# Optimization experiments

Measured on AMD Instinct MI355X. Metric: run time of the kernel, lower is better.

## Reference

```python
import jax, jax.numpy as jnp
import numpy as np

B, T, C, H, D, G, V, M = 4, 1024, 768, 12, 4, 4, 32000, 1024
S = C // H


def layernorm(x, g, b, eps=1e-5):
    mu = jnp.mean(x, -1, keepdims=True)
    var = jnp.mean(jnp.square(x - mu), -1, keepdims=True)
    return (x - mu) * jax.lax.rsqrt(var + eps) * g + b


def setup_inputs() -> dict:
    key = jax.random.key(0)
    ks = jax.random.split(key, 12)
    std = 0.02  # matches _init_weights normal(0, 0.02)
    n = lambda k, sh: jax.random.normal(k, sh, jnp.float32) * std
    return {
        'x': jax.random.randint(ks[0], (B, T), 0, V),
        'y': jax.random.randint(ks[1], (B, T), 0, V),
        'wordemb': n(ks[2], (V, C)),
        'posemb': n(ks[3], (M, C)),
        'Wq': n(ks[4], (D, C, C)),
        'Wk': n(ks[5], (D, C, C)),
        'Wv': n(ks[6], (D, C, C)),
        'Wo': n(ks[7], (D, C, C)),
        'bo': jnp.zeros((D, C), jnp.float32),
        'ln1_g': jnp.ones((D, C), jnp.float32),
        'ln1_b': jnp.zeros((D, C), jnp.float32),
        'W1': n(ks[8], (D, C, G * C)),
        'b1': jnp.zeros((D, G * C), jnp.float32),
        'W2': n(ks[9], (D, G * C, C)),
        'b2': jnp.zeros((D, C), jnp.float32),
        'ln2_g': jnp.ones((D, C), jnp.float32),
        'ln2_b': jnp.zeros((D, C), jnp.float32),
        'Wl': n(ks[10], (C, V)),
        'bl': jnp.zeros((V,), jnp.float32),
    }


def _forward(x, y, wordemb, posemb, Wq, Wk, Wv, Wo, bo, ln1_g, ln1_b,
             W1, b1, W2, b2, ln2_g, ln2_b, Wl, bl):
    b, t = x.shape
    emb = wordemb[x] + posemb[:t][None, :, :]  # (b,t,c)
    causal = jnp.tril(jnp.ones((t, t), bool))

    def block(h_in, p):
        wq, wk, wv, wo, bo_, g1, be1, w1, b1_, w2, b2_, g2, be2 = p
        q = (h_in @ wq).reshape(b, t, H, S)
        k = (h_in @ wk).reshape(b, t, H, S)
        v = (h_in @ wv).reshape(b, t, H, S)
        # note: original scales by sqrt(channels), NOT sqrt(head_dim)
        w = jnp.einsum('bqhs,bkhs->bhqk', q, k) / jnp.sqrt(jnp.float32(C))
        w = jnp.where(causal, w, -jnp.inf)
        w = jax.nn.softmax(w, axis=-1)
        att = jnp.einsum('bhqk,bkhs->bqhs', w, v).reshape(b, t, C)
        att = att @ wo + bo_
        h1 = h_in + layernorm(att, g1, be1)   # x + norm1(attn(x))
        ff = jax.nn.relu(h1 @ w1 + b1_) @ w2 + b2_
        h2 = h1 + layernorm(ff, g2, be2)      # x + norm2(ff(x)); dropout=0
        return h2, None

    hfin, _ = jax.lax.scan(
        block, emb,
        (Wq, Wk, Wv, Wo, bo, ln1_g, ln1_b, W1, b1, W2, b2, ln2_g, ln2_b))
    logits = hfin @ Wl + bl  # (b,t,v)
    logp = jax.nn.log_softmax(logits, axis=-1)
    nll = -jnp.take_along_axis(logp, y[..., None], axis=-1)[..., 0]
    loss = jnp.mean(nll)
    return logits, loss


def reference(x, y, wordemb, posemb, Wq, Wk, Wv, Wo, bo, ln1_g, ln1_b,
              W1, b1, W2, b2, ln2_g, ln2_b, Wl, bl):
    return _forward(x, y, wordemb, posemb, Wq, Wk, Wv, Wo, bo, ln1_g, ln1_b,
                    W1, b1, W2, b2, ln2_g, ln2_b, Wl, bl)
```

## Files before the change

kernel.cpp:

```cpp
#include <hip/hip_runtime.h>

#define Bn 4
#define Tn 1024
#define Cn 768
#define Hn 12
#define Dn 4
#define Vn 32000
#define BTn (Bn*Tn)
#define NBX 125

typedef __attribute__((ext_vector_type(8))) short short8;
typedef __attribute__((ext_vector_type(4))) float f32x4;

__device__ __forceinline__ unsigned short f2bf(float f) {
  union { float f; unsigned u; } v; v.f = f;
  unsigned r = v.u + 0x7fffu + ((v.u >> 16) & 1u);
  return (unsigned short)(r >> 16);
}

__device__ __forceinline__ void gload_lds16(const void* g, void* l) {
  __builtin_amdgcn_global_load_lds(
      (const __attribute__((address_space(1))) void*)g,
      (__attribute__((address_space(3))) void*)l, 16, 0, 0);
}

__global__ __launch_bounds__(256)
void transpose_bf16_kernel(const float* __restrict__ src0, unsigned short* __restrict__ dst0,
                           int K, int N, size_t sStride, size_t dStride) {
  const float* src = src0 + blockIdx.z * sStride;
  unsigned short* dst = dst0 + blockIdx.z * dStride;
  __shared__ float tile[32][33];
  const int tx = threadIdx.x, ty = threadIdx.y;
  const int n0 = blockIdx.x * 32, k0 = blockIdx.y * 32;
#pragma unroll
  for (int i = 0; i < 4; ++i)
    tile[ty + i*8][tx] = src[(size_t)(k0 + ty + i*8) * N + n0 + tx];
  __syncthreads();
#pragma unroll
  for (int i = 0; i < 4; ++i)
    dst[(size_t)(n0 + ty + i*8) * K + k0 + tx] = f2bf(tile[tx][ty + i*8]);
}

__global__ __launch_bounds__(256)
void embed_kernel(const int* __restrict__ x, const float* __restrict__ wordemb,
                  const float* __restrict__ posemb, float* __restrict__ h,
                  unsigned short* __restrict__ hb) {
  int i4 = blockIdx.x * 256 + threadIdx.x;
  int row = i4 / (Cn/4), c4 = i4 % (Cn/4);
  int t = row & (Tn - 1);
  int tok = x[row];
  float4 a = ((const float4*)wordemb)[(size_t)tok * (Cn/4) + c4];
  float4 p = ((const float4*)posemb)[(size_t)t * (Cn/4) + c4];
  float4 s; s.x = a.x+p.x; s.y = a.y+p.y; s.z = a.z+p.z; s.w = a.w+p.w;
  ((float4*)h)[i4] = s;
  ushort4 u; u.x = f2bf(s.x); u.y = f2bf(s.y); u.z = f2bf(s.z); u.w = f2bf(s.w);
  ((ushort4*)hb)[i4] = u;
}

__global__ __launch_bounds__(256, 2)
void gemm_l(const unsigned short* __restrict__ A, const unsigned short* __restrict__ Bt,
            const float* __restrict__ bias, float* __restrict__ Cf,
            unsigned short* __restrict__ Cb, int M, int N, int K, int relu) {
  __shared__ __align__(16) unsigned short lds[2*16384];
  const int tid = threadIdx.x;
  const int gx = gridDim.x;
  const int flat = blockIdx.x + gx*blockIdx.y;
  const int chq = (gx * gridDim.y) >> 3;
  const int swz = (flat & 7)*chq + (flat >> 3);
  const int by = swz % gx, bx = swz / gx;
  const int lane = tid & 63, w = tid >> 6;
  const int wr = w >> 1, wc = w & 1;
  const int lr = lane & 15, lq = lane >> 4;
  const int xm = (lr >> 1) & 3;
  const int sslot = (lane & 3) ^ ((lane >> 3) & 3);
  const int NT = K >> 6;

  f32x4 acc[4][4];
#pragma unroll
  for (int i = 0; i < 4; ++i)
#pragma unroll
    for (int j = 0; j < 4; ++j)
      acc[i][j] = (f32x4){0.f, 0.f, 0.f, 0.f};

  const unsigned short* aS = A  + (size_t)(by*128 + w*16 + (lane>>2))*K + sslot*8;
  const unsigned short* bS = Bt + (size_t)(bx*128 + w*16 + (lane>>2))*K + sslot*8;

  auto stA = [&](int t) {
    unsigned short* d = &lds[(t&1)*16384];
    const int k0 = t*64;
#pragma unroll
    for (int kh = 0; kh < 2; ++kh)
#pragma unroll
      for (int i = 0; i < 2; ++i)
        gload_lds16(aS + k0 + kh*32 + (size_t)i*64*K, d + kh*4096 + (i*64 + w*16)*32);
  };
  auto stB = [&](int t) {
    unsigned short* d = &lds[(t&1)*16384 + 8192];
    const int k0 = t*64;
#pragma unroll
    for (int kh = 0; kh < 2; ++kh)
#pragma unroll
      for (int i = 0; i < 2; ++i)
        gload_lds16(bS + k0 + kh*32 + (size_t)i*64*K, d + kh*4096 + (i*64 + w*16)*32);
  };
  auto rdA = [&](int t, int kh, short8* af) {
    const unsigned short* p = &lds[(t&1)*16384 + kh*4096];
#pragma unroll
    for (int mi = 0; mi < 4; ++mi)
      af[mi] = *(const short8*)&p[(wr*64 + mi*16 + lr)*32 + (lq ^ xm)*8];
  };
  auto rdB = [&](int t, int kh, short8* bf) {
    const unsigned short* p = &lds[(t&1)*16384 + 8192 + kh*4096];
#pragma unroll
    for (int nj = 0; nj < 4; ++nj)
      bf[nj] = *(const short8*)&p[(wc*64 + nj*16 + lr)*32 + (lq ^ xm)*8];
  };

  short8 af0[4], af1[4], bf0[4], bf1[4];
  stA(0); stB(0); stA(1);

  for (int t = 0; t < NT; ++t) {
    if (t + 1 < NT) { asm volatile("s_waitcnt vmcnt(4)" ::: "memory"); }
    else            { asm volatile("s_waitcnt vmcnt(0)" ::: "memory"); }
    __builtin_amdgcn_s_barrier();
    __builtin_amdgcn_sched_barrier(0);
    rdA(t, 0, af0); rdA(t, 1, af1); rdB(t, 0, bf0);
    if (t + 1 < NT) stB(t + 1);
    __builtin_amdgcn_s_barrier();
    __builtin_amdgcn_sched_barrier(0);
    __builtin_amdgcn_s_setprio(1);
#pragma unroll
    for (int i = 0; i < 4; ++i)
#pragma unroll
      for (int j = 0; j < 4; ++j)
        acc[i][j] = __builtin_amdgcn_mfma_f32_16x16x32_bf16(af0[i], bf0[j], acc[i][j], 0, 0, 0);
    __builtin_amdgcn_s_setprio(0);
    __builtin_amdgcn_s_barrier();
    rdB(t, 1, bf1);
    if (t + 2 < NT) stA(t + 2);
    __builtin_amdgcn_s_barrier();
    __builtin_amdgcn_sched_barrier(0);
    __builtin_amdgcn_s_setprio(1);
#pragma unroll
    for (int i = 0; i < 4; ++i)
#pragma unroll
      for (int j = 0; j < 4; ++j)
        acc[i][j] = __builtin_amdgcn_mfma_f32_16x16x32_bf16(af1[i], bf1[j], acc[i][j], 0, 0, 0);
    __builtin_amdgcn_s_setprio(0);
  }

#pragma unroll
  for (int mi = 0; mi < 4; ++mi)
#pragma unroll
    for (int nj = 0; nj < 4; ++nj)
#pragma unroll
      for (int r = 0; r < 4; ++r) {
        int grow = by*128 + wr*64 + mi*16 + lq*4 + r;
        int gcol = bx*128 + wc*64 + nj*16 + lr;
        float v = acc[mi][nj][r];
        if (bias) v += bias[gcol];
        if (relu) v = fmaxf(v, 0.f);
        size_t idx = (size_t)grow * N + gcol;
        if (Cf) Cf[idx] = v;
        if (Cb) Cb[idx] = f2bf(v);
      }
}

__global__ __launch_bounds__(512, 1)
void gemm_vocab(const unsigned short* __restrict__ A, const unsigned short* __restrict__ Bt,
                const float* __restrict__ bias, float* __restrict__ Cf,
                float2* __restrict__ lsepart) {
  constexpr int K = 768, N = Vn, NT = 12;
  __shared__ __align__(16) unsigned short lds[2*32768];
  const int tid = threadIdx.x;
  const int bid = blockIdx.x;
  const int swz = (bid & 7)*250 + (bid >> 3);
  const int by = swz & 15, bx = swz >> 4;
  const int lane = tid & 63, w = tid >> 6;
  const int wr = w >> 2, wc = w & 3;
  const int lr = lane & 15, lq = lane >> 4;
  const int xm = (lr >> 1) & 3;
  const int sslot = (lane & 3) ^ ((lane >> 3) & 3);

  f32x4 accLo[4][4], accHi[4][4];
#pragma unroll
  for (int i = 0; i < 4; ++i)
#pragma unroll
    for (int j = 0; j < 4; ++j) {
      accLo[i][j] = (f32x4){0.f,0.f,0.f,0.f};
      accHi[i][j] = (f32x4){0.f,0.f,0.f,0.f};
    }

  const unsigned short* aS = A  + (size_t)(by*256 + w*16 + (lane>>2))*K + sslot*8;
  const unsigned short* bS = Bt + (size_t)(bx*256 + w*16 + (lane>>2))*K + sslot*8;

  auto stA = [&](int t) {
    unsigned short* d = &lds[(t&1)*32768];
    const int k0 = t*64;
#pragma unroll
    for (int kh = 0; kh < 2; ++kh)
#pragma unroll
      for (int i = 0; i < 2; ++i)
        gload_lds16(aS + k0 + kh*32 + (size_t)i*128*K, d + kh*8192 + (i*128 + w*16)*32);
  };
  auto stB = [&](int t) {
    unsigned short* d = &lds[(t&1)*32768 + 16384];
    const int k0 = t*64;
#pragma unroll
    for (int kh = 0; kh < 2; ++kh)
#pragma unroll
      for (int i = 0; i < 2; ++i)
        gload_lds16(bS + k0 + kh*32 + (size_t)i*128*K, d + kh*8192 + (i*128 + w*16)*32);
  };
  auto rdA = [&](int t, int kh, int mh, short8* af) {
    const unsigned short* p = &lds[(t&1)*32768 + kh*8192];
#pragma unroll
    for (int mi = 0; mi < 4; ++mi)
      af[mi] = *(const short8*)&p[(wr*128 + mh*64 + mi*16 + lr)*32 + (lq ^ xm)*8];
  };
  auto rdB = [&](int t, int kh, short8* bf) {
    const unsigned short* p = &lds[(t&1)*32768 + 16384 + kh*8192];
#pragma unroll
    for (int nj = 0; nj < 4; ++nj)
      bf[nj] = *(const short8*)&p[(wc*64 + nj*16 + lr)*32 + (lq ^ xm)*8];
  };

  short8 aLo0[4], aHi0[4], aLo1[4], aHi1[4], bf0[4], bf1[4];
  stA(0); stB(0); stA(1); stB(1);

  for (int t = 0; t < NT; ++t) {
    if (t + 1 < NT) { asm volatile("s_waitcnt vmcnt(8)" ::: "memory"); }
    else            { asm volatile("s_waitcnt vmcnt(0)" ::: "memory"); }
    __builtin_amdgcn_s_barrier();
    __builtin_amdgcn_sched_barrier(0);
    rdA(t, 0, 0, aLo0); rdA(t, 0, 1, aHi0); rdB(t, 0, bf0);
    __builtin_amdgcn_s_barrier();
    __builtin_amdgcn_sched_barrier(0);
    __builtin_amdgcn_s_setprio(1);
#pragma unroll
    for (int i = 0; i < 4; ++i)
#pragma unroll
      for (int j = 0; j < 4; ++j)
        accLo[i][j] = __builtin_amdgcn_mfma_f32_16x16x32_bf16(aLo0[i], bf0[j], accLo[i][j], 0, 0, 0);
    __builtin_amdgcn_s_setprio(0);
    __builtin_amdgcn_s_barrier();
    rdA(t, 1, 0, aLo1); rdA(t, 1, 1, aHi1);
    __builtin_amdgcn_s_barrier();
    __builtin_amdgcn_sched_barrier(0);
    __builtin_amdgcn_s_setprio(1);
#pragma unroll
    for (int i = 0; i < 4; ++i)
#pragma unroll
      for (int j = 0; j < 4; ++j)
        accHi[i][j] = __builtin_amdgcn_mfma_f32_16x16x32_bf16(aHi0[i], bf0[j], accHi[i][j], 0, 0, 0);
    __builtin_amdgcn_s_setprio(0);
    __builtin_amdgcn_s_barrier();
    rdB(t, 1, bf1);
    if (t + 2 < NT) stA(t + 2);
    __builtin_amdgcn_s_barrier();
    __builtin_amdgcn_sched_barrier(0);
    __builtin_amdgcn_s_setprio(1);
#pragma unroll
    for (int i = 0; i < 4; ++i)
#pragma unroll
      for (int j = 0; j < 4; ++j)
        accLo[i][j] = __builtin_amdgcn_mfma_f32_16x16x32_bf16(aLo1[i], bf1[j], accLo[i][j], 0, 0, 0);
    __builtin_amdgcn_s_setprio(0);
    __builtin_amdgcn_s_barrier();
    if (t + 2 < NT) stB(t + 2);
    __builtin_amdgcn_s_barrier();
    __builtin_amdgcn_sched_barrier(0);
    __builtin_amdgcn_s_setprio(1);
#pragma unroll
    for (int i = 0; i < 4; ++i)
#pragma unroll
      for (int j = 0; j < 4; ++j)
        accHi[i][j] = __builtin_amdgcn_mfma_f32_16x16x32_bf16(aHi1[i], bf1[j], accHi[i][j], 0, 0, 0);
    __builtin_amdgcn_s_setprio(0);
  }

  float2* part = (float2*)lds;
#pragma unroll
  for (int half = 0; half < 2; ++half) {
#pragma unroll
    for (int mi = 0; mi < 4; ++mi)
#pragma unroll
      for (int r = 0; r < 4; ++r) {
        float v[4]; float m = -3.0e38f;
#pragma unroll
        for (int nj = 0; nj < 4; ++nj) {
          int gcol = bx*256 + wc*64 + nj*16 + lr;
          float val = (half ? accHi[mi][nj][r] : accLo[mi][nj][r]) + bias[gcol];
          v[nj] = val;
          m = fmaxf(m, val);
        }
        int prow = wr*128 + half*64 + mi*16 + lq*4 + r;
        int grow = by*256 + prow;
        float* crow = Cf + (size_t)grow * N + bx*256 + wc*64 + lr;
#pragma unroll
        for (int nj = 0; nj < 4; ++nj) crow[nj*16] = v[nj];
        float s = 0.f;
#pragma unroll
        for (int nj = 0; nj < 4; ++nj) s += __expf(v[nj] - m);
#pragma unroll
        for (int mask = 1; mask < 16; mask <<= 1) {
          float m2 = __shfl_xor(m, mask), s2 = __shfl_xor(s, mask);
          float mn = fmaxf(m, m2);
          s = s*__expf(m - mn) + s2*__expf(m2 - mn);
          m = mn;
        }
        if (lr == 0) part[prow*4 + wc] = make_float2(m, s);
      }
  }
  __syncthreads();
  if (tid < 256) {
    float2 p = part[tid*4];
    float m = p.x, s = p.y;
#pragma unroll
    for (int wcc = 1; wcc < 4; ++wcc) {
      float2 p2 = part[tid*4 + wcc];
      float mn = fmaxf(m, p2.x);
      s = s*__expf(m - mn) + p2.y*__expf(p2.x - mn);
      m = mn;
    }
    lsepart[(size_t)(by*256 + tid)*NBX + bx] = make_float2(m, s);
  }
}

__global__ __launch_bounds__(256)
void vT_kernel(const unsigned short* __restrict__ qkvb, unsigned short* __restrict__ vT) {
  const int tb = blockIdx.x, hh = blockIdx.y, b = blockIdx.z;
  const int t = threadIdx.x;
  __shared__ unsigned short tile[64][65];
  const int r = t >> 2, c = t & 3;
  const unsigned short* src = qkvb + (size_t)(b*Tn + tb*64 + r) * 2304 + 1536 + hh*64 + c*16;
  short8 v0 = *(const short8*)src;
  short8 v1 = *(const short8*)(src + 8);
#pragma unroll
  for (int j = 0; j < 8; ++j) { tile[r][c*16 + j] = (unsigned short)v0[j]; tile[r][c*16 + 8 + j] = (unsigned short)v1[j]; }
  __syncthreads();
  unsigned short o[16];
#pragma unroll
  for (int j = 0; j < 16; ++j) o[j] = tile[c*16 + j][r];
  unsigned short* dst = vT + ((size_t)((b*Hn + hh)*64 + r)) * Tn + tb*64 + c*16;
  *(ushort4*)(dst)      = *(ushort4*)&o[0];
  *(ushort4*)(dst + 4)  = *(ushort4*)&o[4];
  *(ushort4*)(dst + 8)  = *(ushort4*)&o[8];
  *(ushort4*)(dst + 12) = *(ushort4*)&o[12];
}

__global__ __launch_bounds__(256)
void attn_mfma_kernel(const unsigned short* __restrict__ qkvb,
                      const unsigned short* __restrict__ vT,
                      unsigned short* __restrict__ attb) {
  const int qb = blockIdx.x, hh = blockIdx.y, b = blockIdx.z;
  const int t = threadIdx.x;
  const int lane = t & 63, w = t >> 6;
  const int lr = lane & 15, lg = lane >> 4;
  const float scale = 0.03608439182435161f;

  __shared__ unsigned short Ks[64*64];
  __shared__ unsigned short Vs[64*64];
  __shared__ unsigned short Ps[4][16][72];

  const unsigned short* qsrc = qkvb + (size_t)(b*Tn + qb*64 + w*16 + lr)*2304 + hh*64 + lg*8;
  short8 qa0 = *(const short8*)(qsrc);
  short8 qa1 = *(const short8*)(qsrc + 32);

  f32x4 acc[4];
#pragma unroll
  for (int dt = 0; dt < 4; ++dt) acc[dt] = (f32x4){0.f,0.f,0.f,0.f};
  float m_run[4], l_run[4];
#pragma unroll
  for (int r = 0; r < 4; ++r) { m_run[r] = -1e30f; l_run[r] = 0.f; }

  const int sr = t >> 2, c2 = t & 3;

  for (int kvb = 0; kvb <= qb; ++kvb) {
    __syncthreads();
    {
      const unsigned short* ksrc = qkvb + (size_t)(b*Tn + kvb*64 + sr)*2304 + 768 + hh*64 + c2*16;
      short8 k0 = *(const short8*)ksrc;
      short8 k1 = *(const short8*)(ksrc + 8);
      const unsigned short* vsrc = vT + ((size_t)((b*Hn + hh)*64 + sr))*Tn + kvb*64 + c2*16;
      short8 vv0 = *(const short8*)vsrc;
      short8 vv1 = *(const short8*)(vsrc + 8);
      int s0 = (2*c2) ^ (sr & 7), s1 = (2*c2 + 1) ^ (sr & 7);
      *(short8*)&Ks[sr*64 + s0*8] = k0;
      *(short8*)&Ks[sr*64 + s1*8] = k1;
      *(short8*)&Vs[sr*64 + s0*8] = vv0;
      *(short8*)&Vs[sr*64 + s1*8] = vv1;
    }
    __syncthreads();

    f32x4 s[4];
#pragma unroll
    for (int kt = 0; kt < 4; ++kt) {
      int krow = kt*16 + lr;
      short8 kf0 = *(const short8*)&Ks[krow*64 + ((0 + lg) ^ (krow & 7))*8];
      short8 kf1 = *(const short8*)&Ks[krow*64 + ((4 + lg) ^ (krow & 7))*8];
      f32x4 a = (f32x4){0.f,0.f,0.f,0.f};
      a = __builtin_amdgcn_mfma_f32_16x16x32_bf16(qa0, kf0, a, 0, 0, 0);
      a = __builtin_amdgcn_mfma_f32_16x16x32_bf16(qa1, kf1, a, 0, 0, 0);
      s[kt] = a;
    }
    const bool diag = (kvb == qb);
#pragma unroll
    for (int kt = 0; kt < 4; ++kt)
#pragma unroll
      for (int r = 0; r < 4; ++r) {
        float v = s[kt][r] * scale;
        if (diag && (kt*16 + lr > w*16 + lg*4 + r)) v = -1e30f;
        s[kt][r] = v;
      }
#pragma unroll
    for (int r = 0; r < 4; ++r) {
      float m = fmaxf(fmaxf(s[0][r], s[1][r]), fmaxf(s[2][r], s[3][r]));
      m = fmaxf(m, __shfl_xor(m, 1));
      m = fmaxf(m, __shfl_xor(m, 2));
      m = fmaxf(m, __shfl_xor(m, 4));
      m = fmaxf(m, __shfl_xor(m, 8));
      float mn = fmaxf(m_run[r], m);
      float corr = __expf(m_run[r] - mn);
      m_run[r] = mn;
      float ps = 0.f;
#pragma unroll
      for (int kt = 0; kt < 4; ++kt) {
        float p = __expf(s[kt][r] - mn);
        s[kt][r] = p;
        ps += p;
      }
      ps += __shfl_xor(ps, 1);
      ps += __shfl_xor(ps, 2);
      ps += __shfl_xor(ps, 4);
      ps += __shfl_xor(ps, 8);
      l_run[r] = l_run[r] * corr + ps;
#pragma unroll
      for (int dt = 0; dt < 4; ++dt) acc[dt][r] *= corr;
    }
#pragma unroll
    for (int kt = 0; kt < 4; ++kt)
#pragma unroll
      for (int r = 0; r < 4; ++r)
        Ps[w][lg*4 + r][kt*16 + lr] = f2bf(s[kt][r]);
    short8 pa0 = *(const short8*)&Ps[w][lr][lg*8];
    short8 pa1 = *(const short8*)&Ps[w][lr][32 + lg*8];
#pragma unroll
    for (int dt = 0; dt < 4; ++dt) {
      int drow = dt*16 + lr;
      short8 vf0 = *(const short8*)&Vs[drow*64 + ((0 + lg) ^ (drow & 7))*8];
      short8 vf1 = *(const short8*)&Vs[drow*64 + ((4 + lg) ^ (drow & 7))*8];
      acc[dt] = __builtin_amdgcn_mfma_f32_16x16x32_bf16(pa0, vf0, acc[dt], 0, 0, 0);
      acc[dt] = __builtin_amdgcn_mfma_f32_16x16x32_bf16(pa1, vf1, acc[dt], 0, 0, 0);
    }
  }

  unsigned short* obase = attb + (size_t)(b*Tn + qb*64 + w*16)*768 + hh*64;
#pragma unroll
  for (int dt = 0; dt < 4; ++dt)
#pragma unroll
    for (int r = 0; r < 4; ++r) {
      float v = acc[dt][r] / l_run[r];
      obase[(size_t)(lg*4 + r)*768 + dt*16 + lr] = f2bf(v);
    }
}

__global__ __launch_bounds__(256)
void ln_res_kernel(const float* __restrict__ x, float* __restrict__ h,
                   unsigned short* __restrict__ hb, const float* __restrict__ g,
                   const float* __restrict__ bb) {
  const int row = blockIdx.x, tid = threadIdx.x;
  const float* xr = x + (size_t)row * Cn;
  float v[3], s1 = 0.f, s2 = 0.f;
#pragma unroll
  for (int j = 0; j < 3; ++j) { v[j] = xr[tid + j*256]; s1 += v[j]; s2 += v[j]*v[j]; }
  __shared__ float r1[256], r2[256];
  r1[tid] = s1; r2[tid] = s2;
  __syncthreads();
  for (int s = 128; s > 0; s >>= 1) {
    if (tid < s) { r1[tid] += r1[tid+s]; r2[tid] += r2[tid+s]; }
    __syncthreads();
  }
  float mu = r1[0] * (1.f/768.f);
  float var = r2[0] * (1.f/768.f) - mu*mu;
  float rs = rsqrtf(var + 1e-5f);
  float* hr = h + (size_t)row * Cn;
  unsigned short* hbr = hb + (size_t)row * Cn;
#pragma unroll
  for (int j = 0; j < 3; ++j) {
    int c = tid + j*256;
    float y = hr[c] + (v[j]-mu)*rs*g[c] + bb[c];
    hr[c] = y;
    hbr[c] = f2bf(y);
  }
}

__global__ __launch_bounds__(128)
void loss_part_kernel(const float2* __restrict__ part, const float* __restrict__ logits,
                      const int* __restrict__ y, float* __restrict__ loss_rows) {
  const int row = blockIdx.x, tid = threadIdx.x;
  float m = -3.0e38f, s = 0.f;
  if (tid < NBX) { float2 p = part[(size_t)row*NBX + tid]; m = p.x; s = p.y; }
#pragma unroll
  for (int mask = 1; mask < 64; mask <<= 1) {
    float m2 = __shfl_xor(m, mask), s2 = __shfl_xor(s, mask);
    float mn = fmaxf(m, m2);
    s = s*__expf(m - mn) + s2*__expf(m2 - mn);
    m = mn;
  }
  __shared__ float mw[2], sw[2];
  if ((tid & 63) == 0) { mw[tid >> 6] = m; sw[tid >> 6] = s; }
  __syncthreads();
  if (tid == 0) {
    float m2 = mw[1], s2 = sw[1];
    float mn = fmaxf(m, m2);
    s = s*__expf(m - mn) + s2*__expf(m2 - mn);
    loss_rows[row] = mn + __logf(s) - logits[(size_t)row*Vn + y[row]];
  }
}

__global__ __launch_bounds__(256)
void loss_reduce_kernel(const float* __restrict__ loss_rows, float* __restrict__ out) {
  const int tid = threadIdx.x;
  float s = 0.f;
  for (int j = 0; j < BTn/256; ++j) s += loss_rows[tid + j*256];
  __shared__ float red[256];
  red[tid] = s; __syncthreads();
  for (int st = 128; st > 0; st >>= 1) {
    if (tid < st) red[tid] += red[tid+st];
    __syncthreads();
  }
  if (tid == 0) out[0] = red[0] * (1.f/(float)BTn);
}

extern "C" void kernel_launch(void* const* d_in, const int* in_sizes, int n_in,
                              void* d_out, int out_size, void* d_ws, size_t ws_size,
                              hipStream_t stream) {
  const int*   x       = (const int*)  d_in[0];
  const int*   y       = (const int*)  d_in[1];
  const float* wordemb = (const float*)d_in[2];
  const float* posemb  = (const float*)d_in[3];
  const float* Wq      = (const float*)d_in[4];
  const float* Wk      = (const float*)d_in[5];
  const float* Wv      = (const float*)d_in[6];
  const float* Wo      = (const float*)d_in[7];
  const float* bo      = (const float*)d_in[8];
  const float* ln1_g   = (const float*)d_in[9];
  const float* ln1_b   = (const float*)d_in[10];
  const float* W1      = (const float*)d_in[11];
  const float* b1      = (const float*)d_in[12];
  const float* W2      = (const float*)d_in[13];
  const float* b2      = (const float*)d_in[14];
  const float* ln2_g   = (const float*)d_in[15];
  const float* ln2_b   = (const float*)d_in[16];
  const float* Wl      = (const float*)d_in[17];
  const float* bl      = (const float*)d_in[18];

  char* ws = (char*)d_ws;
  size_t off = 0;
  auto alloc = [&](size_t bytes) -> char* {
    char* p = ws + off;
    off += (bytes + 255) & ~(size_t)255;
    return p;
  };
  unsigned short* wqkvT = (unsigned short*)alloc((size_t)Dn*2304*768*2);
  unsigned short* woT   = (unsigned short*)alloc((size_t)Dn*768*768*2);
  unsigned short* w1T   = (unsigned short*)alloc((size_t)Dn*3072*768*2);
  unsigned short* w2T   = (unsigned short*)alloc((size_t)Dn*768*3072*2);
  unsigned short* wlT   = (unsigned short*)alloc((size_t)Vn*768*2);
  float*          h     = (float*)alloc((size_t)BTn*Cn*4);
  unsigned short* hb    = (unsigned short*)alloc((size_t)BTn*Cn*2);
  unsigned short* qkvb  = (unsigned short*)alloc((size_t)BTn*3072*2);
  unsigned short* vTb   = (unsigned short*)alloc((size_t)Bn*Hn*64*Tn*2);
  unsigned short* attb  = (unsigned short*)alloc((size_t)BTn*Cn*2);
  float*          tmp   = (float*)alloc((size_t)BTn*Cn*4);
  float*          loss_rows = (float*)alloc((size_t)BTn*4);
  float2*         lsepart   = (float2*)alloc((size_t)BTn*NBX*8);
  unsigned short* ff1b  = qkvb;

  dim3 tb(32, 8);
  transpose_bf16_kernel<<<dim3(24,24,Dn), tb, 0, stream>>>(Wq, wqkvT,             Cn, Cn, (size_t)Cn*Cn, (size_t)2304*768);
  transpose_bf16_kernel<<<dim3(24,24,Dn), tb, 0, stream>>>(Wk, wqkvT + 768*768,   Cn, Cn, (size_t)Cn*Cn, (size_t)2304*768);
  transpose_bf16_kernel<<<dim3(24,24,Dn), tb, 0, stream>>>(Wv, wqkvT + 1536*768,  Cn, Cn, (size_t)Cn*Cn, (size_t)2304*768);
  transpose_bf16_kernel<<<dim3(24,24,Dn), tb, 0, stream>>>(Wo, woT,               Cn, Cn, (size_t)Cn*Cn, (size_t)768*768);
  transpose_bf16_kernel<<<dim3(96,24,Dn), tb, 0, stream>>>(W1, w1T, 768, 3072, (size_t)768*3072, (size_t)3072*768);
  transpose_bf16_kernel<<<dim3(24,96,Dn), tb, 0, stream>>>(W2, w2T, 3072, 768, (size_t)3072*768, (size_t)768*3072);
  transpose_bf16_kernel<<<dim3(1000,24,1), tb, 0, stream>>>(Wl, wlT, 768, Vn, 0, 0);

  embed_kernel<<<(BTn*Cn/4)/256, 256, 0, stream>>>(x, wordemb, posemb, h, hb);

  for (int d = 0; d < Dn; ++d) {
    gemm_l<<<dim3(BTn/128, 2304/128), 256, 0, stream>>>(
        hb, wqkvT + (size_t)d*2304*768, nullptr, nullptr, qkvb, BTn, 2304, 768, 0);
    vT_kernel<<<dim3(Tn/64, Hn, Bn), 256, 0, stream>>>(qkvb, vTb);
    attn_mfma_kernel<<<dim3(Tn/64, Hn, Bn), 256, 0, stream>>>(qkvb, vTb, attb);
    gemm_l<<<dim3(BTn/128, 768/128), 256, 0, stream>>>(
        attb, woT + (size_t)d*768*768, bo + (size_t)d*768, tmp, nullptr, BTn, 768, 768, 0);
    ln_res_kernel<<<BTn, 256, 0, stream>>>(tmp, h, hb, ln1_g + (size_t)d*768, ln1_b + (size_t)d*768);
    gemm_l<<<dim3(BTn/128, 3072/128), 256, 0, stream>>>(
        hb, w1T + (size_t)d*3072*768, b1 + (size_t)d*3072, nullptr, ff1b, BTn, 3072, 768, 1);
    gemm_l<<<dim3(BTn/128, 768/128), 256, 0, stream>>>(
        ff1b, w2T + (size_t)d*768*3072, b2 + (size_t)d*768, tmp, nullptr, BTn, 768, 3072, 0);
    ln_res_kernel<<<BTn, 256, 0, stream>>>(tmp, h, hb, ln2_g + (size_t)d*768, ln2_b + (size_t)d*768);
  }

  float* logits = (float*)d_out;
  gemm_vocab<<<2000, 512, 0, stream>>>(hb, wlT, bl, logits, lsepart);
  loss_part_kernel<<<BTn, 128, 0, stream>>>(lsepart, logits, y, loss_rows);
  loss_reduce_kernel<<<1, 256, 0, stream>>>(loss_rows, logits + (size_t)BTn*Vn);
}
```

Baseline: 1.334 ms.

## Fuse V transpose into QKV GEMM, double-buffer attention KV, warp-per-row layernorm

The QKV GEMM epilogue now writes the V columns straight into the transposed vT layout through an LDS tile, which removes the separate vT_kernel launch and its extra read and write of V. The attention kernel double-buffers its K/V shared-memory tiles so the next block's loads are issued before the current block's compute, keeping one barrier per iteration. The layernorm-residual kernel now handles one row per wavefront with float4 loads and shuffle reductions instead of a shared-memory tree reduction. Costs: more LDS in attention, and a strided transpose store in the GEMM epilogue.

```diff
diff --git a/kernel.cpp b/kernel.cpp
--- a/kernel.cpp
+++ b/kernel.cpp
@@ -60,7 +60,8 @@
 __global__ __launch_bounds__(256, 2)
 void gemm_l(const unsigned short* __restrict__ A, const unsigned short* __restrict__ Bt,
             const float* __restrict__ bias, float* __restrict__ Cf,
-            unsigned short* __restrict__ Cb, int M, int N, int K, int relu) {
+            unsigned short* __restrict__ Cb, int M, int N, int K, int relu,
+            unsigned short* __restrict__ vTp) {
   __shared__ __align__(16) unsigned short lds[2*16384];
   const int tid = threadIdx.x;
   const int gx = gridDim.x;
@@ -149,21 +150,48 @@
     __builtin_amdgcn_s_setprio(0);
   }
 
-#pragma unroll
-  for (int mi = 0; mi < 4; ++mi)
-#pragma unroll
-    for (int nj = 0; nj < 4; ++nj)
-#pragma unroll
-      for (int r = 0; r < 4; ++r) {
-        int grow = by*128 + wr*64 + mi*16 + lq*4 + r;
-        int gcol = bx*128 + wc*64 + nj*16 + lr;
-        float v = acc[mi][nj][r];
-        if (bias) v += bias[gcol];
-        if (relu) v = fmaxf(v, 0.f);
-        size_t idx = (size_t)grow * N + gcol;
-        if (Cf) Cf[idx] = v;
-        if (Cb) Cb[idx] = f2bf(v);
-      }
+  const bool isV = (vTp != nullptr) && (bx*128 >= 1536);
+  if (!isV) {
+#pragma unroll
+    for (int mi = 0; mi < 4; ++mi)
+#pragma unroll
+      for (int nj = 0; nj < 4; ++nj)
+#pragma unroll
+        for (int r = 0; r < 4; ++r) {
+          int grow = by*128 + wr*64 + mi*16 + lq*4 + r;
+          int gcol = bx*128 + wc*64 + nj*16 + lr;
+          float v = acc[mi][nj][r];
+          if (bias) v += bias[gcol];
+          if (relu) v = fmaxf(v, 0.f);
+          size_t idx = (size_t)grow * N + gcol;
+          if (Cf) Cf[idx] = v;
+          if (Cb) Cb[idx] = f2bf(v);
+        }
+  } else {
+    __syncthreads();
+    unsigned short (*tile)[136] = (unsigned short (*)[136])lds;
+#pragma unroll
+    for (int mi = 0; mi < 4; ++mi)
+#pragma unroll
+      for (int nj = 0; nj < 4; ++nj)
+#pragma unroll
+        for (int r = 0; r < 4; ++r) {
+          int lt = wr*64 + mi*16 + lq*4 + r;
+          int ld = wc*64 + nj*16 + lr;
+          tile[ld][lt] = f2bf(acc[mi][nj][r]);
+        }
+    __syncthreads();
+    const int bq = (by*128) >> 10;
+    const int t0 = (by*128) & 1023;
+#pragma unroll
+    for (int i = 0; i < 32; ++i) {
+      int ld = w*32 + i;
+      int gd = bx*128 + ld - 1536;
+      int hh2 = gd >> 6, dd = gd & 63;
+      ushort2 val = *(ushort2*)&tile[ld][2*lane];
+      *(ushort2*)&vTp[((size_t)((bq*Hn + hh2)*64 + dd))*Tn + t0 + 2*lane] = val;
+    }
+  }
 }
 
 __global__ __launch_bounds__(512, 1)
@@ -328,28 +356,6 @@
 }
 
 __global__ __launch_bounds__(256)
-void vT_kernel(const unsigned short* __restrict__ qkvb, unsigned short* __restrict__ vT) {
-  const int tb = blockIdx.x, hh = blockIdx.y, b = blockIdx.z;
-  const int t = threadIdx.x;
-  __shared__ unsigned short tile[64][65];
-  const int r = t >> 2, c = t & 3;
-  const unsigned short* src = qkvb + (size_t)(b*Tn + tb*64 + r) * 2304 + 1536 + hh*64 + c*16;
-  short8 v0 = *(const short8*)src;
-  short8 v1 = *(const short8*)(src + 8);
-#pragma unroll
-  for (int j = 0; j < 8; ++j) { tile[r][c*16 + j] = (unsigned short)v0[j]; tile[r][c*16 + 8 + j] = (unsigned short)v1[j]; }
-  __syncthreads();
-  unsigned short o[16];
-#pragma unroll
-  for (int j = 0; j < 16; ++j) o[j] = tile[c*16 + j][r];
-  unsigned short* dst = vT + ((size_t)((b*Hn + hh)*64 + r)) * Tn + tb*64 + c*16;
-  *(ushort4*)(dst)      = *(ushort4*)&o[0];
-  *(ushort4*)(dst + 4)  = *(ushort4*)&o[4];
-  *(ushort4*)(dst + 8)  = *(ushort4*)&o[8];
-  *(ushort4*)(dst + 12) = *(ushort4*)&o[12];
-}
-
-__global__ __launch_bounds__(256)
 void attn_mfma_kernel(const unsigned short* __restrict__ qkvb,
                       const unsigned short* __restrict__ vT,
                       unsigned short* __restrict__ attb) {
@@ -359,8 +365,8 @@
   const int lr = lane & 15, lg = lane >> 4;
   const float scale = 0.03608439182435161f;
 
-  __shared__ unsigned short Ks[64*64];
-  __shared__ unsigned short Vs[64*64];
+  __shared__ unsigned short Ks[2][64*64];
+  __shared__ unsigned short Vs[2][64*64];
   __shared__ unsigned short Ps[4][16][72];
 
   const unsigned short* qsrc = qkvb + (size_t)(b*Tn + qb*64 + w*16 + lr)*2304 + hh*64 + lg*8;
@@ -376,29 +382,34 @@
 
   const int sr = t >> 2, c2 = t & 3;
 
+  auto stage = [&](int kvb) {
+    const int buf = kvb & 1;
+    const unsigned short* ksrc = qkvb + (size_t)(b*Tn + kvb*64 + sr)*2304 + 768 + hh*64 + c2*16;
+    short8 k0 = *(const short8*)ksrc;
+    short8 k1 = *(const short8*)(ksrc + 8);
+    const unsigned short* vsrc = vT + ((size_t)((b*Hn + hh)*64 + sr))*Tn + kvb*64 + c2*16;
+    short8 vv0 = *(const short8*)vsrc;
+    short8 vv1 = *(const short8*)(vsrc + 8);
+    int s0 = (2*c2) ^ (sr & 7), s1 = (2*c2 + 1) ^ (sr & 7);
+    *(short8*)&Ks[buf][sr*64 + s0*8] = k0;
+    *(short8*)&Ks[buf][sr*64 + s1*8] = k1;
+    *(short8*)&Vs[buf][sr*64 + s0*8] = vv0;
+    *(short8*)&Vs[buf][sr*64 + s1*8] = vv1;
+  };
+
+  stage(0);
+  __syncthreads();
+
   for (int kvb = 0; kvb <= qb; ++kvb) {
-    __syncthreads();
-    {
-      const unsigned short* ksrc = qkvb + (size_t)(b*Tn + kvb*64 + sr)*2304 + 768 + hh*64 + c2*16;
-      short8 k0 = *(const short8*)ksrc;
-      short8 k1 = *(const short8*)(ksrc + 8);
-      const unsigned short* vsrc = vT + ((size_t)((b*Hn + hh)*64 + sr))*Tn + kvb*64 + c2*16;
-      short8 vv0 = *(const short8*)vsrc;
-      short8 vv1 = *(const short8*)(vsrc + 8);
-      int s0 = (2*c2) ^ (sr & 7), s1 = (2*c2 + 1) ^ (sr & 7);
-      *(short8*)&Ks[sr*64 + s0*8] = k0;
-      *(short8*)&Ks[sr*64 + s1*8] = k1;
-      *(short8*)&Vs[sr*64 + s0*8] = vv0;
-      *(short8*)&Vs[sr*64 + s1*8] = vv1;
-    }
-    __syncthreads();
+    if (kvb < qb) stage(kvb + 1);
+    const int buf = kvb & 1;
 
     f32x4 s[4];
 #pragma unroll
     for (int kt = 0; kt < 4; ++kt) {
       int krow = kt*16 + lr;
-      short8 kf0 = *(const short8*)&Ks[krow*64 + ((0 + lg) ^ (krow & 7))*8];
-      short8 kf1 = *(const short8*)&Ks[krow*64 + ((4 + lg) ^ (krow & 7))*8];
+      short8 kf0 = *(const short8*)&Ks[buf][krow*64 + ((0 + lg) ^ (krow & 7))*8];
+      short8 kf1 = *(const short8*)&Ks[buf][krow*64 + ((4 + lg) ^ (krow & 7))*8];
       f32x4 a = (f32x4){0.f,0.f,0.f,0.f};
       a = __builtin_amdgcn_mfma_f32_16x16x32_bf16(qa0, kf0, a, 0, 0, 0);
       a = __builtin_amdgcn_mfma_f32_16x16x32_bf16(qa1, kf1, a, 0, 0, 0);
@@ -448,11 +459,12 @@
 #pragma unroll
     for (int dt = 0; dt < 4; ++dt) {
       int drow = dt*16 + lr;
-      short8 vf0 = *(const short8*)&Vs[drow*64 + ((0 + lg) ^ (drow & 7))*8];
-      short8 vf1 = *(const short8*)&Vs[drow*64 + ((4 + lg) ^ (drow & 7))*8];
+      short8 vf0 = *(const short8*)&Vs[buf][drow*64 + ((0 + lg) ^ (drow & 7))*8];
+      short8 vf1 = *(const short8*)&Vs[buf][drow*64 + ((4 + lg) ^ (drow & 7))*8];
       acc[dt] = __builtin_amdgcn_mfma_f32_16x16x32_bf16(pa0, vf0, acc[dt], 0, 0, 0);
       acc[dt] = __builtin_amdgcn_mfma_f32_16x16x32_bf16(pa1, vf1, acc[dt], 0, 0, 0);
     }
+    __syncthreads();
   }
 
   unsigned short* obase = attb + (size_t)(b*Tn + qb*64 + w*16)*768 + hh*64;
@@ -469,29 +481,38 @@
 void ln_res_kernel(const float* __restrict__ x, float* __restrict__ h,
                    unsigned short* __restrict__ hb, const float* __restrict__ g,
                    const float* __restrict__ bb) {
-  const int row = blockIdx.x, tid = threadIdx.x;
-  const float* xr = x + (size_t)row * Cn;
-  float v[3], s1 = 0.f, s2 = 0.f;
-#pragma unroll
-  for (int j = 0; j < 3; ++j) { v[j] = xr[tid + j*256]; s1 += v[j]; s2 += v[j]*v[j]; }
-  __shared__ float r1[256], r2[256];
-  r1[tid] = s1; r2[tid] = s2;
-  __syncthreads();
-  for (int s = 128; s > 0; s >>= 1) {
-    if (tid < s) { r1[tid] += r1[tid+s]; r2[tid] += r2[tid+s]; }
-    __syncthreads();
-  }
-  float mu = r1[0] * (1.f/768.f);
-  float var = r2[0] * (1.f/768.f) - mu*mu;
+  const int lane = threadIdx.x & 63;
+  const int row = blockIdx.x*4 + (threadIdx.x >> 6);
+  const float4* xr4 = (const float4*)(x + (size_t)row * Cn);
+  float4 v[3];
+  float s1 = 0.f, s2 = 0.f;
+#pragma unroll
+  for (int j = 0; j < 3; ++j) {
+    v[j] = xr4[lane + j*64];
+    s1 += v[j].x + v[j].y + v[j].z + v[j].w;
+    s2 += v[j].x*v[j].x + v[j].y*v[j].y + v[j].z*v[j].z + v[j].w*v[j].w;
+  }
+#pragma unroll
+  for (int m = 1; m < 64; m <<= 1) { s1 += __shfl_xor(s1, m); s2 += __shfl_xor(s2, m); }
+  float mu = s1 * (1.f/768.f);
+  float var = s2 * (1.f/768.f) - mu*mu;
   float rs = rsqrtf(var + 1e-5f);
-  float* hr = h + (size_t)row * Cn;
-  unsigned short* hbr = hb + (size_t)row * Cn;
+  float4* hr4 = (float4*)(h + (size_t)row * Cn);
+  ushort4* hb4 = (ushort4*)(hb + (size_t)row * Cn);
+  const float4* g4 = (const float4*)g;
+  const float4* b4 = (const float4*)bb;
 #pragma unroll
   for (int j = 0; j < 3; ++j) {
-    int c = tid + j*256;
-    float y = hr[c] + (v[j]-mu)*rs*g[c] + bb[c];
-    hr[c] = y;
-    hbr[c] = f2bf(y);
+    int c = lane + j*64;
+    float4 hv = hr4[c], gv = g4[c], bv = b4[c];
+    float4 y;
+    y.x = hv.x + (v[j].x - mu)*rs*gv.x + bv.x;
+    y.y = hv.y + (v[j].y - mu)*rs*gv.y + bv.y;
+    y.z = hv.z + (v[j].z - mu)*rs*gv.z + bv.z;
+    y.w = hv.w + (v[j].w - mu)*rs*gv.w + bv.w;
+    hr4[c] = y;
+    ushort4 u; u.x = f2bf(y.x); u.y = f2bf(y.y); u.z = f2bf(y.z); u.w = f2bf(y.w);
+    hb4[c] = u;
   }
 }
 
@@ -591,17 +612,16 @@
 
   for (int d = 0; d < Dn; ++d) {
     gemm_l<<<dim3(BTn/128, 2304/128), 256, 0, stream>>>(
-        hb, wqkvT + (size_t)d*2304*768, nullptr, nullptr, qkvb, BTn, 2304, 768, 0);
-    vT_kernel<<<dim3(Tn/64, Hn, Bn), 256, 0, stream>>>(qkvb, vTb);
+        hb, wqkvT + (size_t)d*2304*768, nullptr, nullptr, qkvb, BTn, 2304, 768, 0, vTb);
     attn_mfma_kernel<<<dim3(Tn/64, Hn, Bn), 256, 0, stream>>>(qkvb, vTb, attb);
     gemm_l<<<dim3(BTn/128, 768/128), 256, 0, stream>>>(
-        attb, woT + (size_t)d*768*768, bo + (size_t)d*768, tmp, nullptr, BTn, 768, 768, 0);
-    ln_res_kernel<<<BTn, 256, 0, stream>>>(tmp, h, hb, ln1_g + (size_t)d*768, ln1_b + (size_t)d*768);
+        attb, woT + (size_t)d*768*768, bo + (size_t)d*768, tmp, nullptr, BTn, 768, 768, 0, nullptr);
+    ln_res_kernel<<<BTn/4, 256, 0, stream>>>(tmp, h, hb, ln1_g + (size_t)d*768, ln1_b + (size_t)d*768);
     gemm_l<<<dim3(BTn/128, 3072/128), 256, 0, stream>>>(
-        hb, w1T + (size_t)d*3072*768, b1 + (size_t)d*3072, nullptr, ff1b, BTn, 3072, 768, 1);
+        hb, w1T + (size_t)d*3072*768, b1 + (size_t)d*3072, nullptr, ff1b, BTn, 3072, 768, 1, nullptr);
     gemm_l<<<dim3(BTn/128, 768/128), 256, 0, stream>>>(
-        ff1b, w2T + (size_t)d*768*3072, b2 + (size_t)d*768, tmp, nullptr, BTn, 768, 3072, 0);
-    ln_res_kernel<<<BTn, 256, 0, stream>>>(tmp, h, hb, ln2_g + (size_t)d*768, ln2_b + (size_t)d*768);
+        ff1b, w2T + (size_t)d*768*3072, b2 + (size_t)d*768, tmp, nullptr, BTn, 768, 3072, 0, nullptr);
+    ln_res_kernel<<<BTn/4, 256, 0, stream>>>(tmp, h, hb, ln2_g + (size_t)d*768, ln2_b + (size_t)d*768);
   }
 
   float* logits = (float*)d_out;
```

New measurement: 1.304 ms. 1.02x faster.
